# Kernel tuning notes

Hardware: AMD Instinct MI355X
Metric: run time of the kernel (lower is better)

## Reference

```python
import jax, jax.numpy as jnp
import numpy as np

N, E, F_IN, HID, C = 100000, 3200000, 512, 16, 40


def setup_inputs() -> dict:
    key = jax.random.key(0)
    k1, k2, k3, k4 = jax.random.split(key, 4)
    x = jax.random.normal(k1, (N, F_IN), dtype=jnp.float32)
    edge_index = jax.random.randint(k2, (2, E), 0, N, dtype=jnp.int64)
    W1 = jax.random.normal(k3, (F_IN, HID), dtype=jnp.float32) * (1.0 / np.sqrt(F_IN))
    b1 = jnp.zeros((HID,), dtype=jnp.float32)
    W2 = jax.random.normal(k4, (HID, C), dtype=jnp.float32) * (1.0 / np.sqrt(HID))
    b2 = jnp.zeros((C,), dtype=jnp.float32)
    return {"x": x, "edge_index": edge_index, "W1": W1, "b1": b1, "W2": W2, "b2": b2}


def reference(x, edge_index, W1, b1, W2, b2):
    n = x.shape[0]
    # PyG GCNConv: add self-loops, symmetric normalization D^-1/2 (A+I) D^-1/2
    loops = jnp.arange(n, dtype=edge_index.dtype)
    row = jnp.concatenate([edge_index[0], loops])  # source nodes
    col = jnp.concatenate([edge_index[1], loops])  # target nodes
    ones = jnp.ones(row.shape[0], dtype=x.dtype)
    deg = jax.ops.segment_sum(ones, col, num_segments=n)
    dinv = jnp.where(deg > 0, jax.lax.rsqrt(deg), 0.0).astype(x.dtype)
    norm = dinv[row] * dinv[col]  # [E+N]

    def gcn_conv(h, W, b):
        h = h @ W                                   # linear transform first (small out dim)
        msg = h[row] * norm[:, None]                # gather + scale
        agg = jax.ops.segment_sum(msg, col, num_segments=n)  # scatter-add
        return agg + b

    h = jax.nn.relu(gcn_conv(x, W1, b1))
    # dropout is identity in eval mode (F.dropout(training=self.training))
    out = gcn_conv(h, W2, b2)
    return jax.nn.log_softmax(out, axis=1)
```

## Files before the change

kernel.cpp:

```cpp
#include <hip/hip_runtime.h>
#include <hip/hip_fp16.h>

#define F_IN 512
#define HID  16
#define NCLS 40
#define KSPL 4
#define KH   (F_IN / KSPL)
#define BSH2 8
#define BNODES 256
#define NBMAX 512
#define EPB 8192
#define CAP 12288

__device__ __forceinline__ float4 ld_h4(const __half* p) {
    uint2 u = *reinterpret_cast<const uint2*>(p);
    __half2 a = *reinterpret_cast<__half2*>(&u.x);
    __half2 b = *reinterpret_cast<__half2*>(&u.y);
    float2 fa = __half22float2(a), fb = __half22float2(b);
    return make_float4(fa.x, fa.y, fb.x, fb.y);
}

__device__ __forceinline__ void st_h4(__half* p, float4 v) {
    __half2 a = __floats2half2_rn(v.x, v.y);
    __half2 b = __floats2half2_rn(v.z, v.w);
    uint2 u;
    u.x = *reinterpret_cast<unsigned*>(&a);
    u.y = *reinterpret_cast<unsigned*>(&b);
    *reinterpret_cast<uint2*>(p) = u;
}

__global__ __launch_bounds__(512) void k_front(
    const int* __restrict__ col, int* __restrict__ lhists,
    const float* __restrict__ x, const float* __restrict__ W1,
    float* __restrict__ yp4, int ne, int n, int neb, int gblk) {
    __shared__ int lh[NBMAX];
    int t = threadIdx.x;
    if (blockIdx.x < neb) {
        lh[t] = 0;
        __syncthreads();
        int base = blockIdx.x * EPB;
        int end = min(ne, base + EPB);
        int e = base + t * 4;
        for (; e + 3 < end; e += 2048) {
            int4 c = *reinterpret_cast<const int4*>(col + e);
            atomicAdd(&lh[c.x >> BSH2], 1);
            atomicAdd(&lh[c.y >> BSH2], 1);
            atomicAdd(&lh[c.z >> BSH2], 1);
            atomicAdd(&lh[c.w >> BSH2], 1);
        }
        for (; e < end; ++e) atomicAdd(&lh[col[e] >> BSH2], 1);
        __syncthreads();
        lhists[(size_t)blockIdx.x * NBMAX + t] = lh[t];
        return;
    }
    int fb = blockIdx.x - neb;
    int part = fb / gblk;
    int node = (fb % gblk) * 512 + t;
    if (node >= n) return;
    const float* xr = x + (size_t)node * F_IN + part * KH;
    const float* Wb = W1 + (size_t)part * KH * HID;
    float acc[HID];
#pragma unroll
    for (int j = 0; j < HID; ++j) acc[j] = 0.f;
#define STEP(av, kk) \
    _Pragma("unroll") for (int j = 0; j < HID; ++j) acc[j] = fmaf(av, w[(kk) * HID + j], acc[j]);
#pragma unroll
    for (int k = 0; k < KH; k += 16) {
        const float4* xv = reinterpret_cast<const float4*>(xr + k);
        float4 a0 = xv[0], a1 = xv[1], a2 = xv[2], a3 = xv[3];
        const float* w = Wb + (size_t)k * HID;
        STEP(a0.x, 0)  STEP(a0.y, 1)  STEP(a0.z, 2)  STEP(a0.w, 3)
        STEP(a1.x, 4)  STEP(a1.y, 5)  STEP(a1.z, 6)  STEP(a1.w, 7)
        STEP(a2.x, 8)  STEP(a2.y, 9)  STEP(a2.z, 10) STEP(a2.w, 11)
        STEP(a3.x, 12) STEP(a3.y, 13) STEP(a3.z, 14) STEP(a3.w, 15)
    }
    float4* o4 = reinterpret_cast<float4*>(yp4 + ((size_t)part * n + node) * HID);
#pragma unroll
    for (int q = 0; q < 4; ++q)
        o4[q] = make_float4(acc[4 * q], acc[4 * q + 1], acc[4 * q + 2], acc[4 * q + 3]);
}

__global__ __launch_bounds__(512) void k_bscan(
    const int* __restrict__ lhists, int* __restrict__ bstart,
    int* __restrict__ bcur, int nb, int neb) {
    __shared__ int sh[512];
    int t = threadIdx.x;
    int s = 0;
#pragma unroll 4
    for (int j = 0; j < neb; ++j) s += lhists[(size_t)j * NBMAX + t];
    int v = (t < nb) ? s : 0;
    sh[t] = v;
    __syncthreads();
    for (int off = 1; off < 512; off <<= 1) {
        int u = (t >= off) ? sh[t - off] : 0;
        __syncthreads();
        sh[t] += u;
        __syncthreads();
    }
    if (t < nb) {
        int ex = sh[t] - v;
        bstart[t] = ex;
        bcur[t] = ex;
    }
    if (t == nb - 1) bstart[nb] = sh[t];
}

__global__ __launch_bounds__(512) void k_bucket(
    const int* __restrict__ row, const int* __restrict__ col,
    const int* __restrict__ lhists, int* __restrict__ bcur,
    int* __restrict__ packed, int ne) {
    __shared__ int lbase[NBMAX];
    __shared__ int gbase[NBMAX];
    __shared__ int lcur[NBMAX];
    __shared__ int buf[EPB];
    __shared__ unsigned short bof[EPB];
    int t = threadIdx.x;
    int own = lhists[(size_t)blockIdx.x * NBMAX + t];
    lcur[t] = 0;
    if (own > 0) gbase[t] = atomicAdd(&bcur[t], own);
    lbase[t] = own;
    __syncthreads();
    for (int off = 1; off < 512; off <<= 1) {
        int v = (t >= off) ? lbase[t - off] : 0;
        __syncthreads();
        lbase[t] += v;
        __syncthreads();
    }
    int ex = lbase[t] - own;
    __syncthreads();
    lbase[t] = ex;
    __syncthreads();
    int base = blockIdx.x * EPB;
    int end = min(ne, base + EPB);
    for (int e = base + t; e < end; e += 512) {
        int r = row[e], c = col[e];
        int gb = c >> BSH2;
        int rk = atomicAdd(&lcur[gb], 1);
        int pos = lbase[gb] + rk;
        buf[pos] = r | ((c & (BNODES - 1)) << 24);
        bof[pos] = (unsigned short)gb;
    }
    __syncthreads();
    int m = end - base;
    for (int k = t; k < m; k += 512) {
        int gb = bof[k];
        packed[gbase[gb] + (k - lbase[gb])] = buf[k];
    }
}

__global__ __launch_bounds__(512) void k_csr(
    int* __restrict__ cnt, const int* __restrict__ bstart,
    const int* __restrict__ packed, int* __restrict__ ptr,
    int* __restrict__ rows_sorted, int n, int nb) {
    __shared__ int sh[BNODES];
    __shared__ int lcur[BNODES];
    __shared__ int lrows[CAP];
    int b = blockIdx.x, t = threadIdx.x;
    int c0 = b << BSH2;
    int nloc = min(BNODES, n - c0);
    int s = bstart[b], e = bstart[b + 1];
    int m = e - s;
    if (t < BNODES) sh[t] = 0;
    __syncthreads();
    for (int k = t; k < m; k += 512)
        atomicAdd(&sh[((unsigned)packed[s + k]) >> 24], 1);
    __syncthreads();
    int own = (t < BNODES) ? sh[t] : 0;
    if (t < nloc) cnt[c0 + t] = own;
    for (int off = 1; off < BNODES; off <<= 1) {
        int v = (t >= off && t < BNODES) ? sh[t - off] : 0;
        __syncthreads();
        if (t < BNODES) sh[t] += v;
        __syncthreads();
    }
    if (t < nloc) {
        int ex = sh[t] - own;
        ptr[c0 + t] = s + ex;
        lcur[t] = ex;
    }
    if (b == nb - 1 && t == 0) ptr[n] = e;
    __syncthreads();
    if (m <= CAP) {
        for (int k = t; k < m; k += 512) {
            int p = packed[s + k];
            int pos = atomicAdd(&lcur[((unsigned)p) >> 24], 1);
            lrows[pos] = p & 0xFFFFFF;
        }
        __syncthreads();
        for (int k = t; k < m; k += 512) rows_sorted[s + k] = lrows[k];
    } else {
        for (int k = t; k < m; k += 512) {
            int p = packed[s + k];
            int pos = atomicAdd(&lcur[((unsigned)p) >> 24], 1);
            rows_sorted[s + pos] = p & 0xFFFFFF;
        }
    }
}

__global__ void k_comb(const float* __restrict__ yp4, const int* __restrict__ cnt,
                       __half* __restrict__ yp, int n) {
    int i = blockIdx.x * blockDim.x + threadIdx.x;
    if (i >= n * 4) return;
    int node = i >> 2;
    float di = rsqrtf((float)(cnt[node] + 1));
    size_t S = (size_t)n * 4;
    const float4* p = reinterpret_cast<const float4*>(yp4);
    float sx = 0.f, sy = 0.f, sz = 0.f, sw = 0.f;
#pragma unroll
    for (int s = 0; s < KSPL; ++s) {
        float4 a = p[i + s * S];
        sx += a.x; sy += a.y; sz += a.z; sw += a.w;
    }
    st_h4(yp + (size_t)i * 4, make_float4(di * sx, di * sy, di * sz, di * sw));
}

template <bool RELU>
__global__ void k_agg(const int* __restrict__ ptr, const int* __restrict__ rows_sorted,
                      const __half* __restrict__ src, const int* __restrict__ cnt,
                      const float* __restrict__ b1,
                      __half* __restrict__ dst_h, float* __restrict__ dst_f, int n) {
    int t = blockIdx.x * blockDim.x + threadIdx.x;
    int g = t >> 2;
    if (g >= n) return;
    int q = (t & 3) << 2;
    float4 acc = ld_h4(src + (size_t)g * HID + q);
    int s = ptr[g], e2 = ptr[g + 1];
    int k = s;
    for (; k + 3 < e2; k += 4) {
        int r0 = rows_sorted[k],     r1 = rows_sorted[k + 1];
        int r2 = rows_sorted[k + 2], r3 = rows_sorted[k + 3];
        float4 v0 = ld_h4(src + (size_t)r0 * HID + q);
        float4 v1 = ld_h4(src + (size_t)r1 * HID + q);
        float4 v2 = ld_h4(src + (size_t)r2 * HID + q);
        float4 v3 = ld_h4(src + (size_t)r3 * HID + q);
        acc.x += (v0.x + v1.x) + (v2.x + v3.x);
        acc.y += (v0.y + v1.y) + (v2.y + v3.y);
        acc.z += (v0.z + v1.z) + (v2.z + v3.z);
        acc.w += (v0.w + v1.w) + (v2.w + v3.w);
    }
    for (; k < e2; ++k) {
        int r0 = rows_sorted[k];
        float4 v0 = ld_h4(src + (size_t)r0 * HID + q);
        acc.x += v0.x; acc.y += v0.y; acc.z += v0.z; acc.w += v0.w;
    }
    float d = rsqrtf((float)(cnt[g] + 1));
    if (RELU) {
        float4 bb = *reinterpret_cast<const float4*>(b1 + q);
        float4 o;
        o.x = d * fmaxf(fmaf(d, acc.x, bb.x), 0.f);
        o.y = d * fmaxf(fmaf(d, acc.y, bb.y), 0.f);
        o.z = d * fmaxf(fmaf(d, acc.z, bb.z), 0.f);
        o.w = d * fmaxf(fmaf(d, acc.w, bb.w), 0.f);
        st_h4(dst_h + (size_t)g * HID + q, o);
    } else {
        float4 o = make_float4(d * acc.x, d * acc.y, d * acc.z, d * acc.w);
        *reinterpret_cast<float4*>(dst_f + (size_t)g * HID + q) = o;
    }
}

__global__ void k_final(const float* __restrict__ agg2, const float* __restrict__ W2,
                        const float* __restrict__ b2, float* __restrict__ out, int n) {
    int node = blockIdx.x * blockDim.x + threadIdx.x;
    if (node >= n) return;
    const float4* ar = reinterpret_cast<const float4*>(agg2 + (size_t)node * HID);
    float a[HID];
#pragma unroll
    for (int q = 0; q < 4; ++q) {
        float4 t = ar[q];
        a[4 * q] = t.x; a[4 * q + 1] = t.y; a[4 * q + 2] = t.z; a[4 * q + 3] = t.w;
    }
    float z[NCLS];
#pragma unroll
    for (int j = 0; j < NCLS; ++j) z[j] = b2[j];
#pragma unroll
    for (int i = 0; i < HID; ++i) {
        const float* w = W2 + (size_t)i * NCLS;
        float ai = a[i];
#pragma unroll
        for (int j = 0; j < NCLS; ++j) z[j] = fmaf(ai, w[j], z[j]);
    }
    float m = z[0];
#pragma unroll
    for (int j = 1; j < NCLS; ++j) m = fmaxf(m, z[j]);
    float s = 0.f;
#pragma unroll
    for (int j = 0; j < NCLS; ++j) s += __expf(z[j] - m);
    float ls = m + __logf(s);
    float* o = out + (size_t)node * NCLS;
#pragma unroll
    for (int q = 0; q < NCLS / 4; ++q)
        *reinterpret_cast<float4*>(o + 4 * q) =
            make_float4(z[4 * q] - ls, z[4 * q + 1] - ls, z[4 * q + 2] - ls, z[4 * q + 3] - ls);
}

extern "C" void kernel_launch(void* const* d_in, const int* in_sizes, int n_in,
                              void* d_out, int out_size, void* d_ws, size_t ws_size,
                              hipStream_t stream) {
    const float* x  = (const float*)d_in[0];
    const int*   ei = (const int*)d_in[1];
    const float* W1 = (const float*)d_in[2];
    const float* b1 = (const float*)d_in[3];
    const float* W2 = (const float*)d_in[4];
    const float* b2 = (const float*)d_in[5];
    float* out = (float*)d_out;

    const int N = in_sizes[0] / F_IN;
    const int E = in_sizes[1] / 2;
    const int* row = ei;
    const int* col = ei + E;
    const int NBUCK = (N + BNODES - 1) >> BSH2;
    const int NEB = (E + EPB - 1) / EPB;
    const int GBLK = (N + 511) >> 9;

    char* w = (char*)d_ws;
    int*   cnt    = (int*)w;   w += (size_t)N * 4;
    int*   bstart = (int*)w;   w += (size_t)(NBMAX + 1) * 4;
    int*   bcur   = (int*)w;   w += (size_t)NBMAX * 4;
    int*   lhists = (int*)w;   w += (size_t)NEB * NBMAX * 4;
    int*   ptr    = (int*)w;   w += (size_t)(N + 1) * 4;
    int*   rows_sorted = (int*)w; w += (size_t)E * 4;
    int*   packed = (int*)w;   w += (size_t)E * 4;
    float* yp4    = (float*)w; w += (size_t)KSPL * N * HID * 4;
    __half* yp_h  = (__half*)w; w += (size_t)N * HID * 2;
    __half* hp_h  = (__half*)w; w += (size_t)N * HID * 2;
    float* agg2   = (float*)w; w += (size_t)N * HID * 4;

    const int B = 256;
    k_front <<<NEB + KSPL * GBLK, 512, 0, stream>>>(col, lhists, x, W1, yp4, E, N, NEB, GBLK);
    k_bscan <<<1, 512, 0, stream>>>(lhists, bstart, bcur, NBUCK, NEB);
    k_bucket<<<NEB, 512, 0, stream>>>(row, col, lhists, bcur, packed, E);
    k_csr   <<<NBUCK, 512, 0, stream>>>(cnt, bstart, packed, ptr, rows_sorted, N, NBUCK);
    k_comb  <<<((N * 4) + B - 1) / B, B, 0, stream>>>(yp4, cnt, yp_h, N);
    k_agg<true> <<<((N * 4) + B - 1) / B, B, 0, stream>>>(ptr, rows_sorted, yp_h, cnt, b1, hp_h, nullptr, N);
    k_agg<false><<<((N * 4) + B - 1) / B, B, 0, stream>>>(ptr, rows_sorted, hp_h, cnt, nullptr, nullptr, agg2, N);
    k_final <<<(N + B - 1) / B, B, 0, stream>>>(agg2, W2, b2, out, N);
}
```

Measured before the change: 231.6 us.

## Fuse second aggregation with output layer and store split-K partials in fp16

```diff
diff --git a/kernel.cpp b/kernel.cpp
--- a/kernel.cpp
+++ b/kernel.cpp
@@ -32,7 +32,7 @@
 __global__ __launch_bounds__(512) void k_front(
     const int* __restrict__ col, int* __restrict__ lhists,
     const float* __restrict__ x, const float* __restrict__ W1,
-    float* __restrict__ yp4, int ne, int n, int neb, int gblk) {
+    __half* __restrict__ yp4, int ne, int n, int neb, int gblk) {
     __shared__ int lh[NBMAX];
     int t = threadIdx.x;
     if (blockIdx.x < neb) {
@@ -74,10 +74,10 @@
         STEP(a2.x, 8)  STEP(a2.y, 9)  STEP(a2.z, 10) STEP(a2.w, 11)
         STEP(a3.x, 12) STEP(a3.y, 13) STEP(a3.z, 14) STEP(a3.w, 15)
     }
-    float4* o4 = reinterpret_cast<float4*>(yp4 + ((size_t)part * n + node) * HID);
+    __half* o = yp4 + ((size_t)part * n + node) * HID;
 #pragma unroll
     for (int q = 0; q < 4; ++q)
-        o4[q] = make_float4(acc[4 * q], acc[4 * q + 1], acc[4 * q + 2], acc[4 * q + 3]);
+        st_h4(o + q * 4, make_float4(acc[4 * q], acc[4 * q + 1], acc[4 * q + 2], acc[4 * q + 3]));
 }
 
 __global__ __launch_bounds__(512) void k_bscan(
@@ -197,28 +197,25 @@
     }
 }
 
-__global__ void k_comb(const float* __restrict__ yp4, const int* __restrict__ cnt,
+__global__ void k_comb(const __half* __restrict__ yp4, const int* __restrict__ cnt,
                        __half* __restrict__ yp, int n) {
     int i = blockIdx.x * blockDim.x + threadIdx.x;
     if (i >= n * 4) return;
     int node = i >> 2;
     float di = rsqrtf((float)(cnt[node] + 1));
-    size_t S = (size_t)n * 4;
-    const float4* p = reinterpret_cast<const float4*>(yp4);
+    size_t S = (size_t)n * HID;
     float sx = 0.f, sy = 0.f, sz = 0.f, sw = 0.f;
 #pragma unroll
     for (int s = 0; s < KSPL; ++s) {
-        float4 a = p[i + s * S];
+        float4 a = ld_h4(yp4 + s * S + (size_t)i * 4);
         sx += a.x; sy += a.y; sz += a.z; sw += a.w;
     }
     st_h4(yp + (size_t)i * 4, make_float4(di * sx, di * sy, di * sz, di * sw));
 }
 
-template <bool RELU>
-__global__ void k_agg(const int* __restrict__ ptr, const int* __restrict__ rows_sorted,
-                      const __half* __restrict__ src, const int* __restrict__ cnt,
-                      const float* __restrict__ b1,
-                      __half* __restrict__ dst_h, float* __restrict__ dst_f, int n) {
+__global__ void k_agg1(const int* __restrict__ ptr, const int* __restrict__ rows_sorted,
+                       const __half* __restrict__ src, const int* __restrict__ cnt,
+                       const float* __restrict__ b1, __half* __restrict__ dst, int n) {
     int t = blockIdx.x * blockDim.x + threadIdx.x;
     int g = t >> 2;
     if (g >= n) return;
@@ -226,17 +223,23 @@
     float4 acc = ld_h4(src + (size_t)g * HID + q);
     int s = ptr[g], e2 = ptr[g + 1];
     int k = s;
-    for (; k + 3 < e2; k += 4) {
+    for (; k + 7 < e2; k += 8) {
         int r0 = rows_sorted[k],     r1 = rows_sorted[k + 1];
         int r2 = rows_sorted[k + 2], r3 = rows_sorted[k + 3];
+        int r4 = rows_sorted[k + 4], r5 = rows_sorted[k + 5];
+        int r6 = rows_sorted[k + 6], r7 = rows_sorted[k + 7];
         float4 v0 = ld_h4(src + (size_t)r0 * HID + q);
         float4 v1 = ld_h4(src + (size_t)r1 * HID + q);
         float4 v2 = ld_h4(src + (size_t)r2 * HID + q);
         float4 v3 = ld_h4(src + (size_t)r3 * HID + q);
-        acc.x += (v0.x + v1.x) + (v2.x + v3.x);
-        acc.y += (v0.y + v1.y) + (v2.y + v3.y);
-        acc.z += (v0.z + v1.z) + (v2.z + v3.z);
-        acc.w += (v0.w + v1.w) + (v2.w + v3.w);
+        float4 v4 = ld_h4(src + (size_t)r4 * HID + q);
+        float4 v5 = ld_h4(src + (size_t)r5 * HID + q);
+        float4 v6 = ld_h4(src + (size_t)r6 * HID + q);
+        float4 v7 = ld_h4(src + (size_t)r7 * HID + q);
+        acc.x += ((v0.x + v1.x) + (v2.x + v3.x)) + ((v4.x + v5.x) + (v6.x + v7.x));
+        acc.y += ((v0.y + v1.y) + (v2.y + v3.y)) + ((v4.y + v5.y) + (v6.y + v7.y));
+        acc.z += ((v0.z + v1.z) + (v2.z + v3.z)) + ((v4.z + v5.z) + (v6.z + v7.z));
+        acc.w += ((v0.w + v1.w) + (v2.w + v3.w)) + ((v4.w + v5.w) + (v6.w + v7.w));
     }
     for (; k < e2; ++k) {
         int r0 = rows_sorted[k];
@@ -244,53 +247,76 @@
         acc.x += v0.x; acc.y += v0.y; acc.z += v0.z; acc.w += v0.w;
     }
     float d = rsqrtf((float)(cnt[g] + 1));
-    if (RELU) {
-        float4 bb = *reinterpret_cast<const float4*>(b1 + q);
-        float4 o;
-        o.x = d * fmaxf(fmaf(d, acc.x, bb.x), 0.f);
-        o.y = d * fmaxf(fmaf(d, acc.y, bb.y), 0.f);
-        o.z = d * fmaxf(fmaf(d, acc.z, bb.z), 0.f);
-        o.w = d * fmaxf(fmaf(d, acc.w, bb.w), 0.f);
-        st_h4(dst_h + (size_t)g * HID + q, o);
-    } else {
-        float4 o = make_float4(d * acc.x, d * acc.y, d * acc.z, d * acc.w);
-        *reinterpret_cast<float4*>(dst_f + (size_t)g * HID + q) = o;
-    }
-}
-
-__global__ void k_final(const float* __restrict__ agg2, const float* __restrict__ W2,
-                        const float* __restrict__ b2, float* __restrict__ out, int n) {
-    int node = blockIdx.x * blockDim.x + threadIdx.x;
-    if (node >= n) return;
-    const float4* ar = reinterpret_cast<const float4*>(agg2 + (size_t)node * HID);
-    float a[HID];
-#pragma unroll
-    for (int q = 0; q < 4; ++q) {
-        float4 t = ar[q];
-        a[4 * q] = t.x; a[4 * q + 1] = t.y; a[4 * q + 2] = t.z; a[4 * q + 3] = t.w;
-    }
+    float4 bb = *reinterpret_cast<const float4*>(b1 + q);
+    float4 o;
+    o.x = d * fmaxf(fmaf(d, acc.x, bb.x), 0.f);
+    o.y = d * fmaxf(fmaf(d, acc.y, bb.y), 0.f);
+    o.z = d * fmaxf(fmaf(d, acc.z, bb.z), 0.f);
+    o.w = d * fmaxf(fmaf(d, acc.w, bb.w), 0.f);
+    st_h4(dst + (size_t)g * HID + q, o);
+}
+
+__global__ void k_agg_final(const int* __restrict__ ptr, const int* __restrict__ rows_sorted,
+                            const __half* __restrict__ src, const int* __restrict__ cnt,
+                            const float* __restrict__ W2, const float* __restrict__ b2,
+                            float* __restrict__ out, int n) {
+    int t = blockIdx.x * blockDim.x + threadIdx.x;
+    int g = t >> 2;
+    if (g >= n) return;
+    int q = (t & 3) << 2;
+    float4 acc = ld_h4(src + (size_t)g * HID + q);
+    int s = ptr[g], e2 = ptr[g + 1];
+    int k = s;
+    for (; k + 7 < e2; k += 8) {
+        int r0 = rows_sorted[k],     r1 = rows_sorted[k + 1];
+        int r2 = rows_sorted[k + 2], r3 = rows_sorted[k + 3];
+        int r4 = rows_sorted[k + 4], r5 = rows_sorted[k + 5];
+        int r6 = rows_sorted[k + 6], r7 = rows_sorted[k + 7];
+        float4 v0 = ld_h4(src + (size_t)r0 * HID + q);
+        float4 v1 = ld_h4(src + (size_t)r1 * HID + q);
+        float4 v2 = ld_h4(src + (size_t)r2 * HID + q);
+        float4 v3 = ld_h4(src + (size_t)r3 * HID + q);
+        float4 v4 = ld_h4(src + (size_t)r4 * HID + q);
+        float4 v5 = ld_h4(src + (size_t)r5 * HID + q);
+        float4 v6 = ld_h4(src + (size_t)r6 * HID + q);
+        float4 v7 = ld_h4(src + (size_t)r7 * HID + q);
+        acc.x += ((v0.x + v1.x) + (v2.x + v3.x)) + ((v4.x + v5.x) + (v6.x + v7.x));
+        acc.y += ((v0.y + v1.y) + (v2.y + v3.y)) + ((v4.y + v5.y) + (v6.y + v7.y));
+        acc.z += ((v0.z + v1.z) + (v2.z + v3.z)) + ((v4.z + v5.z) + (v6.z + v7.z));
+        acc.w += ((v0.w + v1.w) + (v2.w + v3.w)) + ((v4.w + v5.w) + (v6.w + v7.w));
+    }
+    for (; k < e2; ++k) {
+        int r0 = rows_sorted[k];
+        float4 v0 = ld_h4(src + (size_t)r0 * HID + q);
+        acc.x += v0.x; acc.y += v0.y; acc.z += v0.z; acc.w += v0.w;
+    }
+    float d = rsqrtf((float)(cnt[g] + 1));
+    float h0 = d * acc.x, h1 = d * acc.y, h2 = d * acc.z, h3 = d * acc.w;
+    const float* w0 = W2 + (size_t)(q + 0) * NCLS;
+    const float* w1 = W2 + (size_t)(q + 1) * NCLS;
+    const float* w2 = W2 + (size_t)(q + 2) * NCLS;
+    const float* w3 = W2 + (size_t)(q + 3) * NCLS;
     float z[NCLS];
 #pragma unroll
-    for (int j = 0; j < NCLS; ++j) z[j] = b2[j];
-#pragma unroll
-    for (int i = 0; i < HID; ++i) {
-        const float* w = W2 + (size_t)i * NCLS;
-        float ai = a[i];
-#pragma unroll
-        for (int j = 0; j < NCLS; ++j) z[j] = fmaf(ai, w[j], z[j]);
-    }
+    for (int j = 0; j < NCLS; ++j)
+        z[j] = fmaf(h0, w0[j], fmaf(h1, w1[j], fmaf(h2, w2[j], h3 * w3[j])));
+#pragma unroll
+    for (int j = 0; j < NCLS; ++j) z[j] += __shfl_xor(z[j], 1, 64);
+#pragma unroll
+    for (int j = 0; j < NCLS; ++j) z[j] += __shfl_xor(z[j], 2, 64);
+#pragma unroll
+    for (int j = 0; j < NCLS; ++j) z[j] += b2[j];
     float m = z[0];
 #pragma unroll
     for (int j = 1; j < NCLS; ++j) m = fmaxf(m, z[j]);
-    float s = 0.f;
-#pragma unroll
-    for (int j = 0; j < NCLS; ++j) s += __expf(z[j] - m);
-    float ls = m + __logf(s);
-    float* o = out + (size_t)node * NCLS;
-#pragma unroll
-    for (int q = 0; q < NCLS / 4; ++q)
-        *reinterpret_cast<float4*>(o + 4 * q) =
-            make_float4(z[4 * q] - ls, z[4 * q + 1] - ls, z[4 * q + 2] - ls, z[4 * q + 3] - ls);
+    float ssum = 0.f;
+#pragma unroll
+    for (int j = 0; j < NCLS; ++j) ssum += __expf(z[j] - m);
+    float ls = m + __logf(ssum);
+    int qq = t & 3;
+    float* o = out + (size_t)g * NCLS + qq * 10;
+#pragma unroll
+    for (int j = 0; j < 10; ++j) o[j] = z[qq * 10 + j] - ls;
 }
 
 extern "C" void kernel_launch(void* const* d_in, const int* in_sizes, int n_in,
@@ -320,10 +346,9 @@
     int*   ptr    = (int*)w;   w += (size_t)(N + 1) * 4;
     int*   rows_sorted = (int*)w; w += (size_t)E * 4;
     int*   packed = (int*)w;   w += (size_t)E * 4;
-    float* yp4    = (float*)w; w += (size_t)KSPL * N * HID * 4;
+    __half* yp4   = (__half*)w; w += (size_t)KSPL * N * HID * 2;
     __half* yp_h  = (__half*)w; w += (size_t)N * HID * 2;
     __half* hp_h  = (__half*)w; w += (size_t)N * HID * 2;
-    float* agg2   = (float*)w; w += (size_t)N * HID * 4;
 
     const int B = 256;
     k_front <<<NEB + KSPL * GBLK, 512, 0, stream>>>(col, lhists, x, W1, yp4, E, N, NEB, GBLK);
@@ -331,7 +356,6 @@
     k_bucket<<<NEB, 512, 0, stream>>>(row, col, lhists, bcur, packed, E);
     k_csr   <<<NBUCK, 512, 0, stream>>>(cnt, bstart, packed, ptr, rows_sorted, N, NBUCK);
     k_comb  <<<((N * 4) + B - 1) / B, B, 0, stream>>>(yp4, cnt, yp_h, N);
-    k_agg<true> <<<((N * 4) + B - 1) / B, B, 0, stream>>>(ptr, rows_sorted, yp_h, cnt, b1, hp_h, nullptr, N);
-    k_agg<false><<<((N * 4) + B - 1) / B, B, 0, stream>>>(ptr, rows_sorted, hp_h, cnt, nullptr, nullptr, agg2, N);
-    k_final <<<(N + B - 1) / B, B, 0, stream>>>(agg2, W2, b2, out, N);
-}
+    k_agg1  <<<((N * 4) + B - 1) / B, B, 0, stream>>>(ptr, rows_sorted, yp_h, cnt, b1, hp_h, N);
+    k_agg_final<<<((N * 4) + B - 1) / B, B, 0, stream>>>(ptr, rows_sorted, hp_h, cnt, W2, b2, out, N);
+}
```

Result: slower. 249.1 us (+7.6%).
